# Kernel tuning notes

Hardware: AMD Instinct MI355X
Metric: run time of the kernel (lower is better)

Reference implementation:

```python
import jax, jax.numpy as jnp
import numpy as np

B, L, D, H = 4, 2048, 1024, 16
HD = D // H
EPS = 1e-6
THETA = 10000.0


def _rmsnorm(x, w):
    rms = jax.lax.rsqrt(jnp.mean(x * x, axis=-1, keepdims=True) + EPS)
    return x * rms * w


def _rope(q, k):
    # q,k: [B,H,L,HD]; standard half-split rotary embedding
    pos = jnp.arange(L, dtype=jnp.float32)
    inv_freq = 1.0 / (THETA ** (jnp.arange(0, HD, 2, dtype=jnp.float32) / HD))  # [HD/2]
    ang = pos[:, None] * inv_freq[None, :]                 # [L, HD/2]
    cos = jnp.cos(ang)[None, None]                         # [1,1,L,HD/2]
    sin = jnp.sin(ang)[None, None]

    def rot(t):
        t1, t2 = t[..., : HD // 2], t[..., HD // 2 :]
        return jnp.concatenate([t1 * cos - t2 * sin, t1 * sin + t2 * cos], axis=-1)

    return rot(q), rot(k)


def setup_inputs() -> dict:
    key = jax.random.key(0)
    ks = jax.random.split(key, 4)
    return {
        "x": jax.random.normal(ks[0], (B, L, D), dtype=jnp.float32),
        "Wqkv": jax.random.normal(ks[1], (D, 3 * D), dtype=jnp.float32) * (D ** -0.5),
        "bqkv": jnp.zeros((3 * D,), dtype=jnp.float32),
        "qn_w": jnp.ones((HD,), dtype=jnp.float32),
        "kn_w": jnp.ones((HD,), dtype=jnp.float32),
        "Wout": jax.random.normal(ks[2], (D, D), dtype=jnp.float32) * (D ** -0.5),
        "bout": jnp.zeros((D,), dtype=jnp.float32),
    }


def reference(x, Wqkv, bqkv, qn_w, kn_w, Wout, bout):
    # QKV projection: [B,L,3D] -> [3,B,H,L,HD]
    qkv = (x @ Wqkv + bqkv).reshape(B, L, 3, H, HD).transpose(2, 0, 3, 1, 4)
    q, k, v = qkv[0], qkv[1], qkv[2]
    # QK-RMSNorm over head_dim
    q = _rmsnorm(q, qn_w)
    k = _rmsnorm(k, kn_w)
    # RoPE
    q, k = _rope(q, k)
    # softmax attention
    scale = HD ** -0.5
    attn = jnp.einsum("bhqd,bhkd->bhqk", q, k) * scale
    attn = jax.nn.softmax(attn, axis=-1)
    out = jnp.einsum("bhqk,bhkd->bhqd", attn, v)
    out = out.transpose(0, 2, 1, 3).reshape(B, L, D)
    return out @ Wout + bout
```

## Files before the change

### kernel.cpp

```cpp
#include <hip/hip_runtime.h>
#include <hip/hip_bf16.h>
#include <math.h>


#define NB 4
#define NL 2048
#define ND 1024
#define NH 16
#define NHD 64
#define GM (NB * NL)

typedef _Float16 f16;
typedef _Float16 half4v __attribute__((ext_vector_type(4)));
typedef _Float16 half8v __attribute__((ext_vector_type(8)));
typedef float f32x4 __attribute__((ext_vector_type(4)));

#define MFMA16(a, b, c) __builtin_amdgcn_mfma_f32_16x16x32_f16((a), (b), (c), 0, 0, 0)

__device__ __forceinline__ void gload16(const void* g, void* l) {
  __builtin_amdgcn_global_load_lds((const __attribute__((address_space(1))) void*)g,
                                   (__attribute__((address_space(3))) void*)l, 16, 0, 0);
}

__global__ __launch_bounds__(256) void sctable(float* __restrict__ tbl) {
  const int idx = blockIdx.x * 256 + threadIdx.x;
  const int l = idx >> 5, i = idx & 31;
  const float invf = exp2f(-(float)i * 0.41524101186092029f);
  const float ang = (float)l * invf;
  tbl[idx] = cosf(ang);
  tbl[65536 + idx] = sinf(ang);
}

__global__ __launch_bounds__(256) void presplit(const float* __restrict__ x,
                                                f16* __restrict__ xh,
                                                f16* __restrict__ xl) {
  const size_t i = ((size_t)blockIdx.x * 256 + threadIdx.x) * 4;
  const float4 v = *(const float4*)&x[i];
  half4v h, lo;
  h[0] = (f16)v.x; lo[0] = (f16)(v.x - (float)h[0]);
  h[1] = (f16)v.y; lo[1] = (f16)(v.y - (float)h[1]);
  h[2] = (f16)v.z; lo[2] = (f16)(v.z - (float)h[2]);
  h[3] = (f16)v.w; lo[3] = (f16)(v.w - (float)h[3]);
  *(half4v*)&xh[i] = h;
  *(half4v*)&xl[i] = lo;
}

__global__ __launch_bounds__(256) void transplit(const float* __restrict__ Wsrc,
                                                 f16* __restrict__ Th,
                                                 f16* __restrict__ Tl, int N) {
  __shared__ float t[64][65];
  const int tid = threadIdx.x;
  const int n0 = blockIdx.x * 64, k0 = blockIdx.y * 64;
#pragma unroll
  for (int it = 0; it < 4; ++it) {
    const int e = it * 256 + tid;
    const int r = e >> 4, c4 = (e & 15) << 2;
    const float4 v = *(const float4*)&Wsrc[(size_t)(k0 + r) * N + n0 + c4];
    t[r][c4] = v.x; t[r][c4 + 1] = v.y; t[r][c4 + 2] = v.z; t[r][c4 + 3] = v.w;
  }
  __syncthreads();
#pragma unroll
  for (int it = 0; it < 4; ++it) {
    const int e = it * 256 + tid;
    const int rn = e >> 4, ck = (e & 15) << 2;
    half4v h, lo;
#pragma unroll
    for (int u = 0; u < 4; ++u) {
      const float v = t[ck + u][rn];
      const f16 hv = (f16)v;
      h[u] = hv;
      lo[u] = (f16)(v - (float)hv);
    }
    *(half4v*)&Th[(size_t)(n0 + rn) * 1024 + k0 + ck] = h;
    *(half4v*)&Tl[(size_t)(n0 + rn) * 1024 + k0 + ck] = lo;
  }
}

template <int N, int MODE>
__global__ __launch_bounds__(256) void gemm_split(
    const f16* __restrict__ Ah_g, const f16* __restrict__ Al_g,
    const f16* __restrict__ Bh_g, const f16* __restrict__ Bl_g,
    const float* __restrict__ bias, float* __restrict__ out32,
    f16* __restrict__ qh, f16* __restrict__ ql, f16* __restrict__ kh,
    f16* __restrict__ kl, f16* __restrict__ vth, const float* __restrict__ qw,
    const float* __restrict__ kw, const float* __restrict__ tbl) {
  __shared__ f16 Ah[4096], Al[4096], Bh[4096], Bl[4096];
  const int tid = threadIdx.x;
  const int ln = tid & 63, wv = tid >> 6;
  const int ln15 = ln & 15, q4 = ln >> 4;

  const int nwg = (N / 128) * (GM / 128);
  const int flat = blockIdx.y * gridDim.x + blockIdx.x;
  const int sw = (flat & 7) * (nwg >> 3) + (flat >> 3);
  const int bx = sw % (N / 128), by = sw / (N / 128);
  const int m0 = by * 128, n0 = bx * 128;
  const int wr = wv >> 1, wc = wv & 1;

  f32x4 acc[4][4];
#pragma unroll
  for (int i = 0; i < 4; ++i)
#pragma unroll
    for (int j = 0; j < 4; ++j) acc[i][j] = (f32x4){0.f, 0.f, 0.f, 0.f};

  for (int k0 = 0; k0 < 1024; k0 += 32) {
#pragma unroll
    for (int t = 0; t < 2; ++t) {
      const int f = wv * 2 + t;
      const size_t aoff = (size_t)(m0 + f * 16 + ln15) * 1024 + k0 + q4 * 8;
      const size_t boff = (size_t)(n0 + f * 16 + ln15) * 1024 + k0 + q4 * 8;
      gload16(Ah_g + aoff, &Ah[f * 512]);
      gload16(Al_g + aoff, &Al[f * 512]);
      gload16(Bh_g + boff, &Bh[f * 512]);
      gload16(Bl_g + boff, &Bl[f * 512]);
    }
    __syncthreads();

    half8v a_h[4], a_l[4];
#pragma unroll
    for (int i = 0; i < 4; ++i) {
      a_h[i] = *(half8v*)&Ah[(wr * 4 + i) * 512 + ln * 8];
      a_l[i] = *(half8v*)&Al[(wr * 4 + i) * 512 + ln * 8];
    }
#pragma unroll
    for (int j = 0; j < 4; ++j) {
      const half8v b_h = *(half8v*)&Bh[(wc * 4 + j) * 512 + ln * 8];
      const half8v b_l = *(half8v*)&Bl[(wc * 4 + j) * 512 + ln * 8];
#pragma unroll
      for (int i = 0; i < 4; ++i) {
        acc[i][j] = MFMA16(a_h[i], b_h, acc[i][j]);
        acc[i][j] = MFMA16(a_l[i], b_h, acc[i][j]);
        acc[i][j] = MFMA16(a_h[i], b_l, acc[i][j]);
      }
    }
    __syncthreads();
  }

  const int nc = n0 + wc * 64;
  float bv[4];
#pragma unroll
  for (int j = 0; j < 4; ++j) bv[j] = bias[nc + j * 16 + ln15];

  if constexpr (MODE == 0) {
#pragma unroll
    for (int i = 0; i < 4; ++i) {
      const int m = m0 + wr * 64 + i * 16 + q4 * 4;
#pragma unroll
      for (int j = 0; j < 4; ++j)
#pragma unroll
        for (int r = 0; r < 4; ++r)
          out32[(size_t)(m + r) * N + nc + j * 16 + ln15] = acc[i][j][r] + bv[j];
    }
  } else {
    const int s = nc >> 10;
    const int h = (nc >> 6) & 15;
    if (s == 2) {
#pragma unroll
      for (int i = 0; i < 4; ++i) {
        const int m = m0 + wr * 64 + i * 16 + q4 * 4;
        const int b = m >> 11, l0 = m & (NL - 1);
#pragma unroll
        for (int j = 0; j < 4; ++j) {
          half4v pv;
#pragma unroll
          for (int r = 0; r < 4; ++r) pv[r] = (f16)(acc[i][j][r] + bv[j]);
          *(half4v*)&vth[(size_t)((b * NH + h) * NHD + j * 16 + ln15) * NL + l0] = pv;
        }
      }
    } else {
      const float* nw = (s == 0) ? qw : kw;
      f16* dh = (s == 0) ? qh : kh;
      f16* dl = (s == 0) ? ql : kl;
      const float qsc = (s == 0) ? 0.125f * 1.4426950408889634f : 1.0f;
      float wn[4];
#pragma unroll
      for (int j = 0; j < 4; ++j) wn[j] = nw[j * 16 + ln15];
#pragma unroll
      for (int i = 0; i < 4; ++i) {
        const int m = m0 + wr * 64 + i * 16 + q4 * 4;
        const int b = m >> 11, l0 = m & (NL - 1);
        float vv[4][4];
        float ss[4] = {0.f, 0.f, 0.f, 0.f};
#pragma unroll
        for (int j = 0; j < 4; ++j)
#pragma unroll
          for (int r = 0; r < 4; ++r) {
            vv[j][r] = acc[i][j][r] + bv[j];
            ss[r] += vv[j][r] * vv[j][r];
          }
#pragma unroll
        for (int r = 0; r < 4; ++r) {
          ss[r] += __shfl_xor(ss[r], 1);
          ss[r] += __shfl_xor(ss[r], 2);
          ss[r] += __shfl_xor(ss[r], 4);
          ss[r] += __shfl_xor(ss[r], 8);
          ss[r] = rsqrtf(ss[r] * (1.0f / 64.0f) + 1e-6f);
        }
#pragma unroll
        for (int j = 0; j < 4; ++j)
#pragma unroll
          for (int r = 0; r < 4; ++r) vv[j][r] *= ss[r] * wn[j];
#pragma unroll
        for (int jj = 0; jj < 2; ++jj)
#pragma unroll
          for (int r = 0; r < 4; ++r) {
            const int l = l0 + r;
            const float c = tbl[l * 32 + jj * 16 + ln15];
            const float sn = tbl[65536 + l * 32 + jj * 16 + ln15];
            const float t1 = vv[jj][r], t2 = vv[jj + 2][r];
            vv[jj][r] = t1 * c - t2 * sn;
            vv[jj + 2][r] = t1 * sn + t2 * c;
          }
#pragma unroll
        for (int j = 0; j < 4; ++j)
#pragma unroll
          for (int r = 0; r < 4; ++r) {
            const float val = vv[j][r] * qsc;
            const f16 hv = (f16)val;
            const size_t di = (size_t)((b * NH + h) * NL + l0 + r) * NHD + j * 16 + ln15;
            dh[di] = hv;
            dl[di] = (f16)(val - (float)hv);
          }
      }
    }
  }
}

__global__ __launch_bounds__(256) void flash_mfma(
    const f16* __restrict__ qh, const f16* __restrict__ ql,
    const f16* __restrict__ kh, const f16* __restrict__ kl,
    const f16* __restrict__ vth, f16* __restrict__ Oh, f16* __restrict__ Ol) {
  __shared__ f16 KH[4096], KL[4096], VT[4096];
  __shared__ f16 Pl[4][16][72];
  const int tid = threadIdx.x;
  const int ln = tid & 63, wv = tid >> 6;
  const int ln15 = ln & 15, q4 = ln >> 4;

  const int flat = blockIdx.x;
  const int swz = (flat & 7) * 128 + (flat >> 3);
  const int head = swz >> 4;
  const int qt = swz & 15;
  const int b = head >> 4, h = head & 15;
  const int q0 = qt * 128 + wv * 32;
  const size_t hbase = (size_t)head * NL * NHD;

  half8v qfh[2][2], qfl[2][2];
#pragma unroll
  for (int rf = 0; rf < 2; ++rf)
#pragma unroll
    for (int kb = 0; kb < 2; ++kb) {
      const size_t off = hbase + (size_t)(q0 + rf * 16 + ln15) * NHD + kb * 32 + q4 * 8;
      qfh[rf][kb] = *(const half8v*)&qh[off];
      qfl[rf][kb] = *(const half8v*)&ql[off];
    }

  f32x4 o_[4][2];
  float m_[2], l_[2];
#pragma unroll
  for (int df = 0; df < 4; ++df)
#pragma unroll
    for (int rf = 0; rf < 2; ++rf) o_[df][rf] = (f32x4){0.f, 0.f, 0.f, 0.f};
  m_[0] = m_[1] = -INFINITY;
  l_[0] = l_[1] = 0.f;

  for (int kt = 0; kt < NL / 64; ++kt) {
    const int kv0 = kt * 64;
#pragma unroll
    for (int t = 0; t < 6; ++t) {
      const int f = wv * 6 + t;
      if (f < 8) {
        gload16(kh + hbase + (size_t)(kv0 + (f >> 1) * 16 + ln15) * NHD + (f & 1) * 32 + q4 * 8,
                &KH[f * 512]);
      } else if (f < 16) {
        const int g = f - 8;
        gload16(kl + hbase + (size_t)(kv0 + (g >> 1) * 16 + ln15) * NHD + (g & 1) * 32 + q4 * 8,
                &KL[g * 512]);
      } else {
        const int g = f - 16;
        gload16(vth + (size_t)(head * NHD + (g >> 1) * 16 + ln15) * NL + kv0 + (g & 1) * 32 + q4 * 8,
                &VT[g * 512]);
      }
    }
    __syncthreads();

    f32x4 s_[2][4];
#pragma unroll
    for (int rf = 0; rf < 2; ++rf)
#pragma unroll
      for (int cb = 0; cb < 4; ++cb) s_[rf][cb] = (f32x4){0.f, 0.f, 0.f, 0.f};
#pragma unroll
    for (int cb = 0; cb < 4; ++cb) {
      const half8v kh0 = *(half8v*)&KH[(cb * 2 + 0) * 512 + ln * 8];
      const half8v kh1 = *(half8v*)&KH[(cb * 2 + 1) * 512 + ln * 8];
      const half8v kl0 = *(half8v*)&KL[(cb * 2 + 0) * 512 + ln * 8];
      const half8v kl1 = *(half8v*)&KL[(cb * 2 + 1) * 512 + ln * 8];
#pragma unroll
      for (int rf = 0; rf < 2; ++rf) {
        f32x4 t = s_[rf][cb];
        t = MFMA16(kh0, qfh[rf][0], t);
        t = MFMA16(kh1, qfh[rf][1], t);
        t = MFMA16(kl0, qfh[rf][0], t);
        t = MFMA16(kl1, qfh[rf][1], t);
        t = MFMA16(kh0, qfl[rf][0], t);
        t = MFMA16(kh1, qfl[rf][1], t);
        s_[rf][cb] = t;
      }
    }

#pragma unroll
    for (int rf = 0; rf < 2; ++rf) {
      float pmax = -INFINITY;
#pragma unroll
      for (int cb = 0; cb < 4; ++cb)
#pragma unroll
        for (int r = 0; r < 4; ++r) pmax = fmaxf(pmax, s_[rf][cb][r]);
      pmax = fmaxf(pmax, __shfl_xor(pmax, 16));
      pmax = fmaxf(pmax, __shfl_xor(pmax, 32));
      if (!__all(pmax - m_[rf] <= 8.0f)) {
        const float mn = fmaxf(m_[rf], pmax);
        const float al = exp2f(m_[rf] - mn);
        m_[rf] = mn;
        l_[rf] *= al;
#pragma unroll
        for (int df = 0; df < 4; ++df) o_[df][rf] *= al;
      }
      float rs = 0.f;
#pragma unroll
      for (int cb = 0; cb < 4; ++cb) {
        half4v pk;
#pragma unroll
        for (int r = 0; r < 4; ++r) {
          const float p = exp2f(s_[rf][cb][r] - m_[rf]);
          rs += p;
          pk[r] = (f16)p;
        }
        *(half4v*)&Pl[wv][ln15][cb * 16 + q4 * 4] = pk;
      }
      rs += __shfl_xor(rs, 16);
      rs += __shfl_xor(rs, 32);
      l_[rf] += rs;

#pragma unroll
      for (int ks = 0; ks < 2; ++ks) {
        const half8v pb = *(half8v*)&Pl[wv][ln15][ks * 32 + q4 * 8];
#pragma unroll
        for (int df = 0; df < 4; ++df) {
          const half8v vb = *(half8v*)&VT[(df * 2 + ks) * 512 + ln * 8];
          o_[df][rf] = MFMA16(vb, pb, o_[df][rf]);
        }
      }
    }
    __syncthreads();
  }

#pragma unroll
  for (int rf = 0; rf < 2; ++rf) {
    const float invl = 1.0f / l_[rf];
    const int q = q0 + rf * 16 + ln15;
    const size_t rowb = (size_t)(b * NL + q) * ND + h * 64;
#pragma unroll
    for (int df = 0; df < 4; ++df) {
      half4v oh_, ol_;
#pragma unroll
      for (int r = 0; r < 4; ++r) {
        const float val = o_[df][rf][r] * invl;
        const f16 hv = (f16)val;
        oh_[r] = hv;
        ol_[r] = (f16)(val - (float)hv);
      }
      *(half4v*)&Oh[rowb + df * 16 + q4 * 4] = oh_;
      *(half4v*)&Ol[rowb + df * 16 + q4 * 4] = ol_;
    }
  }
}

extern "C" void kernel_launch(void* const* d_in, const int* in_sizes, int n_in,
                              void* d_out, int out_size, void* d_ws,
                              size_t ws_size, hipStream_t stream) {
  const float* x = (const float*)d_in[0];
  const float* Wqkv = (const float*)d_in[1];
  const float* bqkv = (const float*)d_in[2];
  const float* qn_w = (const float*)d_in[3];
  const float* kn_w = (const float*)d_in[4];
  const float* Wout = (const float*)d_in[5];
  const float* bout = (const float*)d_in[6];
  float* out = (float*)d_out;

  char* wsb = (char*)d_ws;
  f16* qh = (f16*)(wsb);
  f16* ql = (f16*)(wsb + (16u << 20));
  f16* kh = (f16*)(wsb + (32u << 20));
  f16* kl = (f16*)(wsb + (48u << 20));
  f16* vth = (f16*)(wsb + (64u << 20));
  float* tbl = (float*)(wsb + (80u << 20));
  f16* WqTh = (f16*)(wsb + (81u << 20));
  f16* WqTl = (f16*)(wsb + (87u << 20));
  f16* xh = (f16*)(wsb + (93u << 20));
  f16* xl = (f16*)(wsb + (109u << 20));
  f16* Oh = (f16*)(wsb + (81u << 20));
  f16* Ol = (f16*)(wsb + (97u << 20));
  f16* WoTh = (f16*)(wsb + (113u << 20));
  f16* WoTl = (f16*)(wsb + (115u << 20));

  sctable<<<256, 256, 0, stream>>>(tbl);
  transplit<<<dim3(48, 16), 256, 0, stream>>>(Wqkv, WqTh, WqTl, 3 * ND);
  presplit<<<8192, 256, 0, stream>>>(x, xh, xl);

  gemm_split<3 * ND, 1><<<dim3(24, 64), 256, 0, stream>>>(
      xh, xl, WqTh, WqTl, bqkv, nullptr, qh, ql, kh, kl, vth, qn_w, kn_w, tbl);

  transplit<<<dim3(16, 16), 256, 0, stream>>>(Wout, WoTh, WoTl, ND);

  flash_mfma<<<1024, 256, 0, stream>>>(qh, ql, kh, kl, vth, Oh, Ol);

  gemm_split<ND, 0><<<dim3(8, 64), 256, 0, stream>>>(
      Oh, Ol, WoTh, WoTl, bout, out, nullptr, nullptr, nullptr, nullptr,
      nullptr, nullptr, nullptr, nullptr);
}
```

Baseline: 567.3 us.

## Double-buffer LDS tiles in split GEMM and flash attention kernels

Both the split-precision GEMM and the flash attention kernel now keep two LDS buffers. The next K/V or A/B tile is prefetched with global_load_lds while MFMAs run on the current tile, so the load-then-sync stall at the top of each iteration is meant to disappear. The attention kernel also raises wave priority around its MFMA blocks with s_setprio. LDS use per block doubles, which may lower occupancy. With one barrier per iteration, correctness relies on the hardware wait counts making the prefetched tile visible before the next iteration reads it.

```diff
diff --git a/kernel.cpp b/kernel.cpp
--- a/kernel.cpp
+++ b/kernel.cpp
@@ -84,7 +84,7 @@
     f16* __restrict__ qh, f16* __restrict__ ql, f16* __restrict__ kh,
     f16* __restrict__ kl, f16* __restrict__ vth, const float* __restrict__ qw,
     const float* __restrict__ kw, const float* __restrict__ tbl) {
-  __shared__ f16 Ah[4096], Al[4096], Bh[4096], Bl[4096];
+  __shared__ f16 Ah[2][4096], Al[2][4096], Bh[2][4096], Bl[2][4096];
   const int tid = threadIdx.x;
   const int ln = tid & 63, wv = tid >> 6;
   const int ln15 = ln & 15, q4 = ln >> 4;
@@ -96,35 +96,42 @@
   const int m0 = by * 128, n0 = bx * 128;
   const int wr = wv >> 1, wc = wv & 1;
 
-  f32x4 acc[4][4];
-#pragma unroll
-  for (int i = 0; i < 4; ++i)
-#pragma unroll
-    for (int j = 0; j < 4; ++j) acc[i][j] = (f32x4){0.f, 0.f, 0.f, 0.f};
-
-  for (int k0 = 0; k0 < 1024; k0 += 32) {
+  auto stage = [&](int buf, int k0) {
 #pragma unroll
     for (int t = 0; t < 2; ++t) {
       const int f = wv * 2 + t;
       const size_t aoff = (size_t)(m0 + f * 16 + ln15) * 1024 + k0 + q4 * 8;
       const size_t boff = (size_t)(n0 + f * 16 + ln15) * 1024 + k0 + q4 * 8;
-      gload16(Ah_g + aoff, &Ah[f * 512]);
-      gload16(Al_g + aoff, &Al[f * 512]);
-      gload16(Bh_g + boff, &Bh[f * 512]);
-      gload16(Bl_g + boff, &Bl[f * 512]);
-    }
-    __syncthreads();
+      gload16(Ah_g + aoff, &Ah[buf][f * 512]);
+      gload16(Al_g + aoff, &Al[buf][f * 512]);
+      gload16(Bh_g + boff, &Bh[buf][f * 512]);
+      gload16(Bl_g + boff, &Bl[buf][f * 512]);
+    }
+  };
+
+  f32x4 acc[4][4];
+#pragma unroll
+  for (int i = 0; i < 4; ++i)
+#pragma unroll
+    for (int j = 0; j < 4; ++j) acc[i][j] = (f32x4){0.f, 0.f, 0.f, 0.f};
+
+  stage(0, 0);
+  __syncthreads();
+
+  for (int it = 0; it < 32; ++it) {
+    const int cur = it & 1;
+    if (it + 1 < 32) stage(cur ^ 1, (it + 1) * 32);
 
     half8v a_h[4], a_l[4];
 #pragma unroll
     for (int i = 0; i < 4; ++i) {
-      a_h[i] = *(half8v*)&Ah[(wr * 4 + i) * 512 + ln * 8];
-      a_l[i] = *(half8v*)&Al[(wr * 4 + i) * 512 + ln * 8];
+      a_h[i] = *(half8v*)&Ah[cur][(wr * 4 + i) * 512 + ln * 8];
+      a_l[i] = *(half8v*)&Al[cur][(wr * 4 + i) * 512 + ln * 8];
     }
 #pragma unroll
     for (int j = 0; j < 4; ++j) {
-      const half8v b_h = *(half8v*)&Bh[(wc * 4 + j) * 512 + ln * 8];
-      const half8v b_l = *(half8v*)&Bl[(wc * 4 + j) * 512 + ln * 8];
+      const half8v b_h = *(half8v*)&Bh[cur][(wc * 4 + j) * 512 + ln * 8];
+      const half8v b_l = *(half8v*)&Bl[cur][(wc * 4 + j) * 512 + ln * 8];
 #pragma unroll
       for (int i = 0; i < 4; ++i) {
         acc[i][j] = MFMA16(a_h[i], b_h, acc[i][j]);
@@ -229,7 +236,7 @@
     const f16* __restrict__ qh, const f16* __restrict__ ql,
     const f16* __restrict__ kh, const f16* __restrict__ kl,
     const f16* __restrict__ vth, f16* __restrict__ Oh, f16* __restrict__ Ol) {
-  __shared__ f16 KH[4096], KL[4096], VT[4096];
+  __shared__ f16 KH[2][4096], KL[2][4096], VT[2][4096];
   __shared__ f16 Pl[4][16][72];
   const int tid = threadIdx.x;
   const int ln = tid & 63, wv = tid >> 6;
@@ -243,6 +250,25 @@
   const int q0 = qt * 128 + wv * 32;
   const size_t hbase = (size_t)head * NL * NHD;
 
+  auto stage = [&](int buf, int kv0) {
+#pragma unroll
+    for (int t = 0; t < 6; ++t) {
+      const int f = wv * 6 + t;
+      if (f < 8) {
+        gload16(kh + hbase + (size_t)(kv0 + (f >> 1) * 16 + ln15) * NHD + (f & 1) * 32 + q4 * 8,
+                &KH[buf][f * 512]);
+      } else if (f < 16) {
+        const int g = f - 8;
+        gload16(kl + hbase + (size_t)(kv0 + (g >> 1) * 16 + ln15) * NHD + (g & 1) * 32 + q4 * 8,
+                &KL[buf][g * 512]);
+      } else {
+        const int g = f - 16;
+        gload16(vth + (size_t)(head * NHD + (g >> 1) * 16 + ln15) * NL + kv0 + (g & 1) * 32 + q4 * 8,
+                &VT[buf][g * 512]);
+      }
+    }
+  };
+
   half8v qfh[2][2], qfl[2][2];
 #pragma unroll
   for (int rf = 0; rf < 2; ++rf)
@@ -262,37 +288,25 @@
   m_[0] = m_[1] = -INFINITY;
   l_[0] = l_[1] = 0.f;
 
+  stage(0, 0);
+  __syncthreads();
+
   for (int kt = 0; kt < NL / 64; ++kt) {
-    const int kv0 = kt * 64;
-#pragma unroll
-    for (int t = 0; t < 6; ++t) {
-      const int f = wv * 6 + t;
-      if (f < 8) {
-        gload16(kh + hbase + (size_t)(kv0 + (f >> 1) * 16 + ln15) * NHD + (f & 1) * 32 + q4 * 8,
-                &KH[f * 512]);
-      } else if (f < 16) {
-        const int g = f - 8;
-        gload16(kl + hbase + (size_t)(kv0 + (g >> 1) * 16 + ln15) * NHD + (g & 1) * 32 + q4 * 8,
-                &KL[g * 512]);
-      } else {
-        const int g = f - 16;
-        gload16(vth + (size_t)(head * NHD + (g >> 1) * 16 + ln15) * NL + kv0 + (g & 1) * 32 + q4 * 8,
-                &VT[g * 512]);
-      }
-    }
-    __syncthreads();
+    const int cur = kt & 1;
+    if (kt + 1 < NL / 64) stage(cur ^ 1, (kt + 1) * 64);
 
     f32x4 s_[2][4];
 #pragma unroll
     for (int rf = 0; rf < 2; ++rf)
 #pragma unroll
       for (int cb = 0; cb < 4; ++cb) s_[rf][cb] = (f32x4){0.f, 0.f, 0.f, 0.f};
+    __builtin_amdgcn_s_setprio(1);
 #pragma unroll
     for (int cb = 0; cb < 4; ++cb) {
-      const half8v kh0 = *(half8v*)&KH[(cb * 2 + 0) * 512 + ln * 8];
-      const half8v kh1 = *(half8v*)&KH[(cb * 2 + 1) * 512 + ln * 8];
-      const half8v kl0 = *(half8v*)&KL[(cb * 2 + 0) * 512 + ln * 8];
-      const half8v kl1 = *(half8v*)&KL[(cb * 2 + 1) * 512 + ln * 8];
+      const half8v kh0 = *(half8v*)&KH[cur][(cb * 2 + 0) * 512 + ln * 8];
+      const half8v kh1 = *(half8v*)&KH[cur][(cb * 2 + 1) * 512 + ln * 8];
+      const half8v kl0 = *(half8v*)&KL[cur][(cb * 2 + 0) * 512 + ln * 8];
+      const half8v kl1 = *(half8v*)&KL[cur][(cb * 2 + 1) * 512 + ln * 8];
 #pragma unroll
       for (int rf = 0; rf < 2; ++rf) {
         f32x4 t = s_[rf][cb];
@@ -305,6 +319,7 @@
         s_[rf][cb] = t;
       }
     }
+    __builtin_amdgcn_s_setprio(0);
 
 #pragma unroll
     for (int rf = 0; rf < 2; ++rf) {
@@ -339,15 +354,17 @@
       rs += __shfl_xor(rs, 32);
       l_[rf] += rs;
 
+      __builtin_amdgcn_s_setprio(1);
 #pragma unroll
       for (int ks = 0; ks < 2; ++ks) {
         const half8v pb = *(half8v*)&Pl[wv][ln15][ks * 32 + q4 * 8];
 #pragma unroll
         for (int df = 0; df < 4; ++df) {
-          const half8v vb = *(half8v*)&VT[(df * 2 + ks) * 512 + ln * 8];
+          const half8v vb = *(half8v*)&VT[cur][(df * 2 + ks) * 512 + ln * 8];
           o_[df][rf] = MFMA16(vb, pb, o_[df][rf]);
         }
       }
+      __builtin_amdgcn_s_setprio(0);
     }
     __syncthreads();
   }
```

Result: slower. 636.2 us (+12.1%).
